# Kernel tuning notes

Measured on AMD Instinct MI355X. Metric: run time of the kernel, lower is better.

Reference implementation:

```python
import jax, jax.numpy as jnp
import numpy as np

N, D, M = 262144, 64, 256
CLAMP = -1e-9  # clamp_max value for the ray denominator


def setup_inputs() -> dict:
    key = jax.random.key(0)
    kz, kp, ka, kb = jax.random.split(key, 4)
    return {
        "z": jax.random.normal(kz, (N, D), dtype=jnp.float32),
        "pivot": jax.random.normal(kp, (D,), dtype=jnp.float32),
        "At": jax.random.normal(ka, (D, M), dtype=jnp.float32),
        "b": jax.random.normal(kb, (M,), dtype=jnp.float32),
    }


def reference(z, pivot, At, b):
    # sign_arg: [N, M] — signed constraint violation A z - b
    sign_arg = z @ At - b[None, :]
    ind = sign_arg >= 0  # violated constraints
    ray = pivot[None, :] - z  # [N, D] direction toward the interior pivot
    # denominator clamped to <= -1e-9 and detached (constant w.r.t. grads)
    denom = jax.lax.stop_gradient(jnp.minimum(ray @ At, CLAMP))  # [N, M]
    alpha = -sign_arg / denom
    # step size = max over violated constraints (alpha*ind zeros out satisfied ones)
    common_alpha = jnp.max(alpha * ind.astype(alpha.dtype), axis=1)  # [N]
    common_ind = jnp.any(ind, axis=1)  # [N] — move only if some constraint violated
    return z + common_ind[:, None].astype(z.dtype) * (common_alpha[:, None] * ray)
```

## Files before the change

### kernel.cpp

```cpp
#include <hip/hip_runtime.h>

#define DIMK 64
#define MC 256
#define BR 64
#define NROWS 262144
#define NB (NROWS / BR)

#define WS_AT 1024
#define WS_NEED (1024 + 65536)

#define LDS_AH 0
#define LDS_AL 16384
#define LDS_GM 32768

typedef _Float16 half8 __attribute__((ext_vector_type(8)));
typedef float f32x16 __attribute__((ext_vector_type(16)));

__global__ void precompute_c(const float* __restrict__ pivot,
                             const float* __restrict__ At,
                             float* __restrict__ ws) {
    const int t = threadIdx.x;
    float acc = 0.f;
#pragma unroll
    for (int k = 0; k < DIMK; ++k) acc = fmaf(pivot[k], At[k * MC + t], acc);
    ws[t] = acc;
}

__global__ void precompute_at(const float* __restrict__ pivot,
                              const float* __restrict__ At,
                              float* __restrict__ ws) {
    const int t = threadIdx.x;
    const int swz = (t & 3) ^ ((t >> 2) & 3);
    float col[DIMK];
    float acc = 0.f;
#pragma unroll
    for (int k = 0; k < DIMK; ++k) {
        col[k] = At[k * MC + t];
        acc = fmaf(pivot[k], col[k], acc);
    }
    ws[t] = acc;
    char* wsb = (char*)ws;
#pragma unroll
    for (int s = 0; s < 2; ++s) {
#pragma unroll
        for (int kc = 0; kc < 4; ++kc) {
            half8 h, l;
#pragma unroll
            for (int j = 0; j < 8; ++j) {
                const float v = col[s * 32 + kc * 8 + j];
                h[j] = (_Float16)v;
                l[j] = (_Float16)(v - (float)h[j]);
            }
            const int off = t * 64 + ((kc ^ swz) << 4);
            *(half8*)(wsb + WS_AT + s * 32768 + off) = h;
            *(half8*)(wsb + WS_AT + s * 32768 + 16384 + off) = l;
        }
    }
}

template <bool PREAT>
__global__ __launch_bounds__(256, 4)
void fused_constrain_mfma(const float* __restrict__ z,
                          const float* __restrict__ pivot,
                          const float* __restrict__ At,
                          const float* __restrict__ b,
                          const float* __restrict__ ws,
                          float* __restrict__ out) {
    __shared__ __align__(16) char lds[33280];

    const int tid  = threadIdx.x;
    const int lane = tid & 63;
    const int li   = lane & 31;
    const int hi   = lane >> 5;
    const int wid  = tid >> 6;
    const int rg   = wid >> 1;
    const int cg   = wid & 1;
    const int R0   = rg * 32;
    const int colbase = cg * 128;
    const int swz  = (li & 3) ^ ((li >> 2) & 3);
    const int base = blockIdx.x * (BR * DIMK);

    auto stage_at = [&](const int s) {
        if constexpr (PREAT) {
            const char* wsA = (const char*)ws + WS_AT + s * 32768;
#pragma unroll
            for (int p = 0; p < 8; ++p) {
                const int f = p * 256 + tid;
                *(float4*)(lds + f * 16) = *(const float4*)(wsA + f * 16);
            }
        } else {
            const int swzT = (tid & 3) ^ ((tid >> 2) & 3);
#pragma unroll
            for (int kc = 0; kc < 4; ++kc) {
                float v[8];
#pragma unroll
                for (int j = 0; j < 8; ++j)
                    v[j] = At[(s * 32 + kc * 8 + j) * MC + tid];
                half8 h, l;
#pragma unroll
                for (int j = 0; j < 8; ++j) {
                    h[j] = (_Float16)v[j];
                    l[j] = (_Float16)(v[j] - (float)h[j]);
                }
                const int off = tid * 64 + ((kc ^ swzT) << 4);
                *(half8*)(lds + LDS_AH + off) = h;
                *(half8*)(lds + LDS_AL + off) = l;
            }
        }
    };

    float4 zf[8];
    {
        const float* zr = z + base + (R0 + li) * DIMK + hi * 8;
#pragma unroll
        for (int q = 0; q < 4; ++q) {
            const float* p = zr + (q >> 1) * 32 + (q & 1) * 16;
            zf[q * 2 + 0] = *(const float4*)(p);
            zf[q * 2 + 1] = *(const float4*)(p + 4);
        }
    }

    stage_at(0);

    half8 azh[4], azl[4];
    const float* zv = (const float*)zf;
#pragma unroll
    for (int q = 0; q < 4; ++q)
#pragma unroll
        for (int j = 0; j < 8; ++j) {
            const float v = zv[q * 8 + j];
            azh[q][j] = (_Float16)v;
            azl[q][j] = (_Float16)(v - (float)azh[q][j]);
        }

    f32x16 acc[4];
#pragma unroll
    for (int ct = 0; ct < 4; ++ct)
#pragma unroll
        for (int e = 0; e < 16; ++e) acc[ct][e] = 0.f;

    __syncthreads();

#pragma unroll
    for (int ksl = 0; ksl < 2; ++ksl) {
        const int cb = ((ksl * 2 + hi) ^ swz) << 4;
        const half8 ah = azh[ksl], al = azl[ksl];
#pragma unroll
        for (int ct = 0; ct < 4; ++ct) {
            const int off = (colbase + ct * 32 + li) * 64 + cb;
            const half8 bh = *(const half8*)(lds + LDS_AH + off);
            const half8 bl = *(const half8*)(lds + LDS_AL + off);
            acc[ct] = __builtin_amdgcn_mfma_f32_32x32x16_f16(ah, bh, acc[ct], 0, 0, 0);
            acc[ct] = __builtin_amdgcn_mfma_f32_32x32x16_f16(ah, bl, acc[ct], 0, 0, 0);
            acc[ct] = __builtin_amdgcn_mfma_f32_32x32x16_f16(al, bh, acc[ct], 0, 0, 0);
        }
    }
    __syncthreads();

    stage_at(1);
    __syncthreads();

#pragma unroll
    for (int ksl = 0; ksl < 2; ++ksl) {
        const int cb = ((ksl * 2 + hi) ^ swz) << 4;
        const half8 ah = azh[2 + ksl], al = azl[2 + ksl];
#pragma unroll
        for (int ct = 0; ct < 4; ++ct) {
            const int off = (colbase + ct * 32 + li) * 64 + cb;
            const half8 bh = *(const half8*)(lds + LDS_AH + off);
            const half8 bl = *(const half8*)(lds + LDS_AL + off);
            acc[ct] = __builtin_amdgcn_mfma_f32_32x32x16_f16(ah, bh, acc[ct], 0, 0, 0);
            acc[ct] = __builtin_amdgcn_mfma_f32_32x32x16_f16(ah, bl, acc[ct], 0, 0, 0);
            acc[ct] = __builtin_amdgcn_mfma_f32_32x32x16_f16(al, bh, acc[ct], 0, 0, 0);
        }
    }

    float bv[4], cv[4];
#pragma unroll
    for (int ct = 0; ct < 4; ++ct) {
        const int c = colbase + ct * 32 + li;
        bv[ct] = b[c];
        cv[ct] = ws[c];
    }
    float gm[16];
#pragma unroll
    for (int r = 0; r < 16; ++r) gm[r] = 0.f;
#pragma unroll
    for (int ct = 0; ct < 4; ++ct)
#pragma unroll
        for (int r = 0; r < 16; ++r) {
            const float sv = acc[ct][r];
            const float sa = sv - bv[ct];
            const float qd = fmaxf(sv - cv[ct], 1e-9f);
            gm[r] = fmaxf(gm[r], sa * __builtin_amdgcn_rcpf(qd));
        }
#pragma unroll
    for (int r = 0; r < 16; ++r)
#pragma unroll
        for (int off = 1; off < 32; off <<= 1)
            gm[r] = fmaxf(gm[r], __shfl_xor(gm[r], off));

    float* gmbuf = (float*)(lds + LDS_GM);
#pragma unroll
    for (int r = 0; r < 16; ++r) {
        const int row = (r & 3) + 8 * (r >> 2) + 4 * hi;
        if (li == 0) gmbuf[rg * 64 + row * 2 + cg] = gm[r];
    }
    __syncthreads();

    const float2 p2 = *(const float2*)(pivot + 2 * li);
    const int r0 = cg * 8;
#pragma unroll
    for (int rr = 0; rr < 8; ++rr) {
        const int r   = r0 + rr;
        const int row = (r & 3) + 8 * (r >> 2) + 4 * hi;
        const float g = fmaxf(gm[r], gmbuf[rg * 64 + row * 2 + (cg ^ 1)]);
        const int idx = base + (R0 + row) * DIMK + 2 * li;
        const float2 zz = *(const float2*)(z + idx);
        float2 o;
        o.x = fmaf(g, p2.x - zz.x, zz.x);
        o.y = fmaf(g, p2.y - zz.y, zz.y);
        *(float2*)(out + idx) = o;
    }
}

extern "C" void kernel_launch(void* const* d_in, const int* in_sizes, int n_in,
                              void* d_out, int out_size, void* d_ws, size_t ws_size,
                              hipStream_t stream) {
    const float* z     = (const float*)d_in[0];
    const float* pivot = (const float*)d_in[1];
    const float* At    = (const float*)d_in[2];
    const float* b     = (const float*)d_in[3];
    float* ws = (float*)d_ws;
    if (ws_size >= (size_t)WS_NEED) {
        precompute_at<<<dim3(1), dim3(MC), 0, stream>>>(pivot, At, ws);
        fused_constrain_mfma<true><<<dim3(NB), dim3(256), 0, stream>>>(
            z, pivot, At, b, ws, (float*)d_out);
    } else {
        precompute_c<<<dim3(1), dim3(MC), 0, stream>>>(pivot, At, ws);
        fused_constrain_mfma<false><<<dim3(NB), dim3(256), 0, stream>>>(
            z, pivot, At, b, ws, (float*)d_out);
    }
}
```

Before: 152.6 us.

## Read At fragments directly from global and stage z tile in LDS for epilogue

```diff
diff --git a/kernel.cpp b/kernel.cpp
--- a/kernel.cpp
+++ b/kernel.cpp
@@ -12,6 +12,8 @@
 #define LDS_AH 0
 #define LDS_AL 16384
 #define LDS_GM 32768
+#define LDS_ZT 0
+#define LDS_GM2 16384
 
 typedef _Float16 half8 __attribute__((ext_vector_type(8)));
 typedef float f32x16 __attribute__((ext_vector_type(16)));
@@ -30,7 +32,6 @@
                               const float* __restrict__ At,
                               float* __restrict__ ws) {
     const int t = threadIdx.x;
-    const int swz = (t & 3) ^ ((t >> 2) & 3);
     float col[DIMK];
     float acc = 0.f;
 #pragma unroll
@@ -39,7 +40,7 @@
         acc = fmaf(pivot[k], col[k], acc);
     }
     ws[t] = acc;
-    char* wsb = (char*)ws;
+    char* wsb = (char*)ws + WS_AT + t * 256;
 #pragma unroll
     for (int s = 0; s < 2; ++s) {
 #pragma unroll
@@ -51,9 +52,8 @@
                 h[j] = (_Float16)v;
                 l[j] = (_Float16)(v - (float)h[j]);
             }
-            const int off = t * 64 + ((kc ^ swz) << 4);
-            *(half8*)(wsb + WS_AT + s * 32768 + off) = h;
-            *(half8*)(wsb + WS_AT + s * 32768 + 16384 + off) = l;
+            *(half8*)(wsb + s * 128 + kc * 32) = h;
+            *(half8*)(wsb + s * 128 + kc * 32 + 16) = l;
         }
     }
 }
@@ -77,37 +77,7 @@
     const int cg   = wid & 1;
     const int R0   = rg * 32;
     const int colbase = cg * 128;
-    const int swz  = (li & 3) ^ ((li >> 2) & 3);
     const int base = blockIdx.x * (BR * DIMK);
-
-    auto stage_at = [&](const int s) {
-        if constexpr (PREAT) {
-            const char* wsA = (const char*)ws + WS_AT + s * 32768;
-#pragma unroll
-            for (int p = 0; p < 8; ++p) {
-                const int f = p * 256 + tid;
-                *(float4*)(lds + f * 16) = *(const float4*)(wsA + f * 16);
-            }
-        } else {
-            const int swzT = (tid & 3) ^ ((tid >> 2) & 3);
-#pragma unroll
-            for (int kc = 0; kc < 4; ++kc) {
-                float v[8];
-#pragma unroll
-                for (int j = 0; j < 8; ++j)
-                    v[j] = At[(s * 32 + kc * 8 + j) * MC + tid];
-                half8 h, l;
-#pragma unroll
-                for (int j = 0; j < 8; ++j) {
-                    h[j] = (_Float16)v[j];
-                    l[j] = (_Float16)(v[j] - (float)h[j]);
-                }
-                const int off = tid * 64 + ((kc ^ swzT) << 4);
-                *(half8*)(lds + LDS_AH + off) = h;
-                *(half8*)(lds + LDS_AL + off) = l;
-            }
-        }
-    };
 
     float4 zf[8];
     {
@@ -120,7 +90,35 @@
         }
     }
 
-    stage_at(0);
+    if constexpr (PREAT) {
+        const int zrow = R0 + li;
+        const int rx = zrow & 15;
+        char* zt = lds + LDS_ZT + zrow * 256;
+#pragma unroll
+        for (int q = 0; q < 4; ++q) {
+            const int c0 = hi * 2 + (q >> 1) * 8 + (q & 1) * 4;
+            *(float4*)(zt + ((c0 ^ rx) << 4))       = zf[q * 2 + 0];
+            *(float4*)(zt + (((c0 + 1) ^ rx) << 4)) = zf[q * 2 + 1];
+        }
+    } else {
+        const int swzT = (tid & 3) ^ ((tid >> 2) & 3);
+#pragma unroll
+        for (int kc = 0; kc < 4; ++kc) {
+            float v[8];
+#pragma unroll
+            for (int j = 0; j < 8; ++j)
+                v[j] = At[(kc * 8 + j) * MC + tid];
+            half8 h, l;
+#pragma unroll
+            for (int j = 0; j < 8; ++j) {
+                h[j] = (_Float16)v[j];
+                l[j] = (_Float16)(v[j] - (float)h[j]);
+            }
+            const int off = tid * 64 + ((kc ^ swzT) << 4);
+            *(half8*)(lds + LDS_AH + off) = h;
+            *(half8*)(lds + LDS_AL + off) = l;
+        }
+    }
 
     half8 azh[4], azl[4];
     const float* zv = (const float*)zf;
@@ -139,39 +137,75 @@
 #pragma unroll
         for (int e = 0; e < 16; ++e) acc[ct][e] = 0.f;
 
-    __syncthreads();
-
-#pragma unroll
-    for (int ksl = 0; ksl < 2; ++ksl) {
-        const int cb = ((ksl * 2 + hi) ^ swz) << 4;
-        const half8 ah = azh[ksl], al = azl[ksl];
-#pragma unroll
-        for (int ct = 0; ct < 4; ++ct) {
-            const int off = (colbase + ct * 32 + li) * 64 + cb;
-            const half8 bh = *(const half8*)(lds + LDS_AH + off);
-            const half8 bl = *(const half8*)(lds + LDS_AL + off);
-            acc[ct] = __builtin_amdgcn_mfma_f32_32x32x16_f16(ah, bh, acc[ct], 0, 0, 0);
-            acc[ct] = __builtin_amdgcn_mfma_f32_32x32x16_f16(ah, bl, acc[ct], 0, 0, 0);
-            acc[ct] = __builtin_amdgcn_mfma_f32_32x32x16_f16(al, bh, acc[ct], 0, 0, 0);
-        }
-    }
-    __syncthreads();
-
-    stage_at(1);
-    __syncthreads();
-
-#pragma unroll
-    for (int ksl = 0; ksl < 2; ++ksl) {
-        const int cb = ((ksl * 2 + hi) ^ swz) << 4;
-        const half8 ah = azh[2 + ksl], al = azl[2 + ksl];
-#pragma unroll
-        for (int ct = 0; ct < 4; ++ct) {
-            const int off = (colbase + ct * 32 + li) * 64 + cb;
-            const half8 bh = *(const half8*)(lds + LDS_AH + off);
-            const half8 bl = *(const half8*)(lds + LDS_AL + off);
-            acc[ct] = __builtin_amdgcn_mfma_f32_32x32x16_f16(ah, bh, acc[ct], 0, 0, 0);
-            acc[ct] = __builtin_amdgcn_mfma_f32_32x32x16_f16(ah, bl, acc[ct], 0, 0, 0);
-            acc[ct] = __builtin_amdgcn_mfma_f32_32x32x16_f16(al, bh, acc[ct], 0, 0, 0);
+    if constexpr (PREAT) {
+        const char* p[4];
+#pragma unroll
+        for (int ct = 0; ct < 4; ++ct)
+            p[ct] = (const char*)ws + WS_AT +
+                    (colbase + ct * 32 + li) * 256 + hi * 32;
+#pragma unroll
+        for (int s = 0; s < 2; ++s)
+#pragma unroll
+            for (int ksl = 0; ksl < 2; ++ksl) {
+                const half8 ah = azh[s * 2 + ksl], al = azl[s * 2 + ksl];
+#pragma unroll
+                for (int ct = 0; ct < 4; ++ct) {
+                    const half8 bh = *(const half8*)(p[ct] + s * 128 + ksl * 64);
+                    const half8 bl = *(const half8*)(p[ct] + s * 128 + ksl * 64 + 16);
+                    acc[ct] = __builtin_amdgcn_mfma_f32_32x32x16_f16(ah, bh, acc[ct], 0, 0, 0);
+                    acc[ct] = __builtin_amdgcn_mfma_f32_32x32x16_f16(ah, bl, acc[ct], 0, 0, 0);
+                    acc[ct] = __builtin_amdgcn_mfma_f32_32x32x16_f16(al, bh, acc[ct], 0, 0, 0);
+                }
+            }
+    } else {
+        const int swz = (li & 3) ^ ((li >> 2) & 3);
+        __syncthreads();
+#pragma unroll
+        for (int ksl = 0; ksl < 2; ++ksl) {
+            const int cb = ((ksl * 2 + hi) ^ swz) << 4;
+            const half8 ah = azh[ksl], al = azl[ksl];
+#pragma unroll
+            for (int ct = 0; ct < 4; ++ct) {
+                const int off = (colbase + ct * 32 + li) * 64 + cb;
+                const half8 bh = *(const half8*)(lds + LDS_AH + off);
+                const half8 bl = *(const half8*)(lds + LDS_AL + off);
+                acc[ct] = __builtin_amdgcn_mfma_f32_32x32x16_f16(ah, bh, acc[ct], 0, 0, 0);
+                acc[ct] = __builtin_amdgcn_mfma_f32_32x32x16_f16(ah, bl, acc[ct], 0, 0, 0);
+                acc[ct] = __builtin_amdgcn_mfma_f32_32x32x16_f16(al, bh, acc[ct], 0, 0, 0);
+            }
+        }
+        __syncthreads();
+        const int swzT = (tid & 3) ^ ((tid >> 2) & 3);
+#pragma unroll
+        for (int kc = 0; kc < 4; ++kc) {
+            float v[8];
+#pragma unroll
+            for (int j = 0; j < 8; ++j)
+                v[j] = At[(32 + kc * 8 + j) * MC + tid];
+            half8 h, l;
+#pragma unroll
+            for (int j = 0; j < 8; ++j) {
+                h[j] = (_Float16)v[j];
+                l[j] = (_Float16)(v[j] - (float)h[j]);
+            }
+            const int off = tid * 64 + ((kc ^ swzT) << 4);
+            *(half8*)(lds + LDS_AH + off) = h;
+            *(half8*)(lds + LDS_AL + off) = l;
+        }
+        __syncthreads();
+#pragma unroll
+        for (int ksl = 0; ksl < 2; ++ksl) {
+            const int cb = ((ksl * 2 + hi) ^ swz) << 4;
+            const half8 ah = azh[2 + ksl], al = azl[2 + ksl];
+#pragma unroll
+            for (int ct = 0; ct < 4; ++ct) {
+                const int off = (colbase + ct * 32 + li) * 64 + cb;
+                const half8 bh = *(const half8*)(lds + LDS_AH + off);
+                const half8 bl = *(const half8*)(lds + LDS_AL + off);
+                acc[ct] = __builtin_amdgcn_mfma_f32_32x32x16_f16(ah, bh, acc[ct], 0, 0, 0);
+                acc[ct] = __builtin_amdgcn_mfma_f32_32x32x16_f16(ah, bl, acc[ct], 0, 0, 0);
+                acc[ct] = __builtin_amdgcn_mfma_f32_32x32x16_f16(al, bh, acc[ct], 0, 0, 0);
+            }
         }
     }
 
@@ -200,7 +234,7 @@
         for (int off = 1; off < 32; off <<= 1)
             gm[r] = fmaxf(gm[r], __shfl_xor(gm[r], off));
 
-    float* gmbuf = (float*)(lds + LDS_GM);
+    float* gmbuf = (float*)(lds + (PREAT ? LDS_GM2 : LDS_GM));
 #pragma unroll
     for (int r = 0; r < 16; ++r) {
         const int row = (r & 3) + 8 * (r >> 2) + 4 * hi;
@@ -215,12 +249,19 @@
         const int r   = r0 + rr;
         const int row = (r & 3) + 8 * (r >> 2) + 4 * hi;
         const float g = fmaxf(gm[r], gmbuf[rg * 64 + row * 2 + (cg ^ 1)]);
-        const int idx = base + (R0 + row) * DIMK + 2 * li;
-        const float2 zz = *(const float2*)(z + idx);
+        const int zrow = R0 + row;
+        float2 zz;
+        if constexpr (PREAT) {
+            const int byt = LDS_ZT + zrow * 256 +
+                            (((li >> 1) ^ (zrow & 15)) << 4) + (li & 1) * 8;
+            zz = *(const float2*)(lds + byt);
+        } else {
+            zz = *(const float2*)(z + base + zrow * DIMK + 2 * li);
+        }
         float2 o;
         o.x = fmaf(g, p2.x - zz.x, zz.x);
         o.y = fmaf(g, p2.y - zz.y, zz.y);
-        *(float2*)(out + idx) = o;
+        *(float2*)(out + base + zrow * DIMK + 2 * li) = o;
     }
 }
 
```

Result: slower. 196.4 us (+28.7%).
